# Performance work log

Measured on AMD Instinct MI355X. Metric: run time of the kernel, lower is better.

The kernel has to match this reference:

```python
import jax, jax.numpy as jnp
import numpy as np

H, KV, D, WIN = 16, 4, 128, 1024


def _rope(x, cos, sin):
    # x: [B, H, S, D]; cos/sin: [1, 1, S, D//2]
    d = x.shape[-1] // 2
    x1, x2 = x[..., :d], x[..., d:]
    S = x.shape[2]
    c, s = cos[:, :, :S], sin[:, :, :S]
    return jnp.concatenate([x1 * c + x2 * s, -x1 * s + x2 * c], axis=-1)


def _rms_norm(x):
    eps = jnp.finfo(x.dtype).eps
    return x * jax.lax.rsqrt(jnp.mean(jnp.square(x), axis=-1, keepdims=True) + eps)


def setup_inputs() -> dict:
    key = jax.random.key(0)
    ks = jax.random.split(key, 7)
    B, S, E = 2, 2048, 2048
    return {
        "x": jax.random.normal(ks[0], (B, S, E), jnp.float32),
        "cos": jax.random.normal(ks[1], (1, 1, S, D // 2), jnp.float32),
        "sin": jax.random.normal(ks[2], (1, 1, S, D // 2), jnp.float32),
        "Wq": jax.random.normal(ks[3], (H * D, E), jnp.float32) * 0.02,
        "Wk": jax.random.normal(ks[4], (KV * D, E), jnp.float32) * 0.02,
        "Wv": jax.random.normal(ks[5], (KV * D, E), jnp.float32) * 0.02,
        "Wo": jax.random.normal(ks[6], (E, H * D), jnp.float32) * 0.02,
    }


def reference(x, cos, sin, Wq, Wk, Wv, Wo):
    B, S, E = x.shape
    rep = H // KV
    # projections -> [B, heads, S, D]
    q = (x @ Wq.T).reshape(B, S, H, D).transpose(0, 2, 1, 3)
    k = (x @ Wk.T).reshape(B, S, KV, D).transpose(0, 2, 1, 3)
    v = (x @ Wv.T).reshape(B, S, KV, D).transpose(0, 2, 1, 3)
    # GQA: materialize repeated K/V heads (matches repeat_interleave)
    k = jnp.repeat(k, rep, axis=1)
    v = jnp.repeat(v, rep, axis=1)
    # RoPE then QK RMSNorm (no learned scale)
    q = _rms_norm(_rope(q, cos, sin))
    k = _rms_norm(_rope(k, cos, sin))
    scores = jnp.einsum("bhqd,bhkd->bhqk", q, k) * (D ** -0.5)
    # causal & sliding-window mask
    i = jnp.arange(S)[:, None]
    j = jnp.arange(S)[None, :]
    mask = (i >= j) & (jnp.abs(i - j) < WIN)
    scores = jnp.where(mask[None, None], scores, -jnp.inf)
    attn = jax.nn.softmax(scores, axis=-1)
    out = jnp.einsum("bhqk,bhkd->bhqd", attn, v)
    out = out.transpose(0, 2, 1, 3).reshape(B, S, H * D)
    return out @ Wo.T
```

## Files before the change

### kernel.cpp

```cpp
#include <hip/hip_runtime.h>
#include <stdint.h>

using bf16 = __bf16;
typedef __bf16 bf16x8 __attribute__((ext_vector_type(8)));
typedef __bf16 bf16x4 __attribute__((ext_vector_type(4)));
typedef float f32x4 __attribute__((ext_vector_type(4)));

#define H_ 16
#define KV_ 4
#define D_ 128
#define WIN_ 1024
#define B_ 2
#define S_ 2048
#define E_ 2048
#define HD_ 2048

__device__ __forceinline__ void gld_lds16(const void* gptr, void* lptr) {
    __builtin_amdgcn_global_load_lds(
        (__attribute__((address_space(1))) void*)(uintptr_t)gptr,
        (__attribute__((address_space(3))) void*)(uintptr_t)lptr, 16, 0, 0);
}

__global__ __launch_bounds__(256) void cvt_all(const float* __restrict__ x,
                                               const float* __restrict__ wq,
                                               const float* __restrict__ wk,
                                               const float* __restrict__ wv,
                                               const float* __restrict__ wo,
                                               bf16* __restrict__ dst) {
    int i = (blockIdx.x * 256 + threadIdx.x) * 4;
    const float* src;
    int off;
    if (i < 8388608)       { src = x;  off = 0; }
    else if (i < 12582912) { src = wq; off = 8388608; }
    else if (i < 13631488) { src = wk; off = 12582912; }
    else if (i < 14680064) { src = wv; off = 13631488; }
    else                   { src = wo; off = 14680064; }
    const float4 v = *(const float4*)(src + (i - off));
    bf16x4 o = {(bf16)v.x, (bf16)v.y, (bf16)v.z, (bf16)v.w};
    *(bf16x4*)(dst + i) = o;
}


#define SCHED0() __builtin_amdgcn_sched_barrier(0)
#define BAR()                          \
    do {                               \
        SCHED0();                      \
        __builtin_amdgcn_s_barrier();  \
        SCHED0();                      \
    } while (0)
#define WAITV(N) asm volatile("s_waitcnt vmcnt(" #N ")" ::: "memory")

#define MMA16(MH, NHI, BF)                                                          \
    do {                                                                            \
        __builtin_amdgcn_s_setprio(1);                                              \
        _Pragma("unroll") for (int kh_ = 0; kh_ < 2; ++kh_) {                       \
            _Pragma("unroll") for (int i_ = 0; i_ < 4; ++i_) {                      \
                _Pragma("unroll") for (int j_ = 0; j_ < 2; ++j_) {                  \
                    acc[(MH) * 4 + i_][(NHI) * 2 + j_] =                            \
                        __builtin_amdgcn_mfma_f32_16x16x32_bf16(                    \
                            af[i_][kh_], BF[j_][kh_],                               \
                            acc[(MH) * 4 + i_][(NHI) * 2 + j_], 0, 0, 0);           \
                }                                                                   \
            }                                                                       \
        }                                                                           \
        __builtin_amdgcn_s_setprio(0);                                              \
    } while (0)

#define TILE_NH2(TT, AC, BC, DOST, WC)                              \
    do {                                                            \
        rdA(AC, 0);                                                 \
        rdB(BC, 0, bf0);                                            \
        rdB(BC, 1, bf1);                                            \
        MMA16(0, 0, bf0);                                           \
        MMA16(0, 1, bf1);                                           \
        rdA(AC, 1);                                                 \
        MMA16(1, 0, bf0);                                           \
        MMA16(1, 1, bf1);                                           \
        BAR();                                                      \
        if (DOST) { stB((TT) + 2, BC); stA((TT) + 2, AC); }         \
        if ((WC) == 8) WAITV(8);                                    \
        else if ((WC) == 0) WAITV(0);                               \
        BAR();                                                      \
    } while (0)

#define TILE_NH1(TT, AC, BC, DOST, WC)                              \
    do {                                                            \
        rdA(AC, 0);                                                 \
        rdB(BC, 0, bf0);                                            \
        MMA16(0, 0, bf0);                                           \
        rdA(AC, 1);                                                 \
        MMA16(1, 0, bf0);                                           \
        BAR();                                                      \
        if (DOST) { stB((TT) + 2, BC); stA((TT) + 2, AC); }         \
        if ((WC) == 6) WAITV(6);                                    \
        else if ((WC) == 0) WAITV(0);                               \
        BAR();                                                      \
    } while (0)

template <int NH>
__device__ __forceinline__ void gemm_core(const bf16* __restrict__ A,
                                          const bf16* __restrict__ W, int K, int m0,
                                          int n0, bf16* sm, f32x4 (&acc)[8][2 * NH]) {
    const int t = threadIdx.x;
    const int lane = t & 63;
    const int wave = t >> 6;
    const int l15 = lane & 15;
    const int quad = lane >> 4;
    const int fsw8 = (l15 & 7) * 8;
    const int wm = (wave & 1) * 128;
    const int wn = (wave >> 1) * (NH * 32);
    const int nt = K >> 6;

    bf16* const As0 = sm;
    bf16* const As1 = sm + 16384;
    bf16* const Bs0 = sm + 32768;
    bf16* const Bs1 = Bs0 + NH * 8192;

    const int su = ((t & 7) ^ ((t >> 3) & 7)) * 8;
    const bf16* Ap = A + (size_t)(m0 + (t >> 3)) * K + su;
    const bf16* Wp = W + (size_t)(n0 + (t >> 3)) * K + su;

    auto stA = [&](int tt, bf16* dst) {
#pragma unroll
        for (int c = 0; c < 4; ++c)
            gld_lds16(Ap + tt * 64 + (size_t)(c * 64) * K, dst + c * 4096 + t * 8);
    };
    auto stB = [&](int tt, bf16* dst) {
#pragma unroll
        for (int c = 0; c < 2 * NH; ++c)
            gld_lds16(Wp + tt * 64 + (size_t)(c * 64) * K, dst + c * 4096 + t * 8);
    };

    bf16x8 af[4][2], bf0[2][2], bf1[2][2];
    auto rdA = [&](const bf16* S, int mh) {
#pragma unroll
        for (int i = 0; i < 4; ++i) {
            const bf16* r = &S[(wm + mh * 64 + i * 16 + l15) * 64];
#pragma unroll
            for (int kh = 0; kh < 2; ++kh)
                af[i][kh] = *(const bf16x8*)&r[((kh * 4 + quad) * 8) ^ fsw8];
        }
    };
    auto rdB = [&](const bf16* S, int nh, bf16x8 (&f)[2][2]) {
#pragma unroll
        for (int j = 0; j < 2; ++j) {
            const bf16* r = &S[(wn + nh * 32 + j * 16 + l15) * 64];
#pragma unroll
            for (int kh = 0; kh < 2; ++kh)
                f[j][kh] = *(const bf16x8*)&r[((kh * 4 + quad) * 8) ^ fsw8];
        }
    };

    stA(0, As0);
    stB(0, Bs0);
    stA(1, As1);
    stB(1, Bs1);
    SCHED0();
    if constexpr (NH == 2) WAITV(8);
    else WAITV(6);
    BAR();

    if constexpr (NH == 2) {
        for (int tt = 0; tt < nt - 2; tt += 2) {
            TILE_NH2(tt, As0, Bs0, 1, 8);
            TILE_NH2(tt + 1, As1, Bs1, 1, 8);
        }
        TILE_NH2(nt - 2, As0, Bs0, 0, 0);
        TILE_NH2(nt - 1, As1, Bs1, 0, -1);
    } else {
        for (int tt = 0; tt < nt - 2; tt += 2) {
            TILE_NH1(tt, As0, Bs0, 1, 6);
            TILE_NH1(tt + 1, As1, Bs1, 1, 6);
        }
        TILE_NH1(nt - 2, As0, Bs0, 0, 0);
        TILE_NH1(nt - 1, As1, Bs1, 0, -1);
    }
}

__global__ __launch_bounds__(512, 2) void gemm_qkv8(const bf16* __restrict__ A,
                                                    const bf16* __restrict__ W,
                                                    const float* __restrict__ cosp,
                                                    const float* __restrict__ sinp,
                                                    bf16* __restrict__ qn,
                                                    bf16* __restrict__ kn,
                                                    bf16* __restrict__ vt) {
    __shared__ alignas(16) bf16 sm[65536];
    const int flat = blockIdx.y * 16 + blockIdx.x;
    const int swz = (flat & 7) * 24 + (flat >> 3);
    const int m0 = (swz & 15) * 256;
    const int n0 = (swz >> 4) * 256;

    f32x4 acc[8][4] = {};
    gemm_core<2>(A, W, E_, m0, n0, sm, acc);

    const int t = threadIdx.x;
    const int lane = t & 63;
    const int wave = t >> 6;
    const int l15 = lane & 15;
    const int quad = lane >> 4;
    const int wm = (wave & 1) * 128;
    const int wn = (wave >> 1) * 64;
    bf16* Cs = sm;

#pragma unroll
    for (int ch = 0; ch < 2; ++ch) {
        __syncthreads();
        if (wm == ch * 128) {
#pragma unroll
            for (int mi = 0; mi < 8; ++mi) {
                const int rl = mi * 16 + quad * 4;
#pragma unroll
                for (int nf = 0; nf < 4; ++nf) {
                    const int col = wn + nf * 16 + l15;
#pragma unroll
                    for (int r = 0; r < 4; ++r)
                        Cs[(rl + r) * 264 + col] = (bf16)acc[mi][nf][r];
                }
            }
        }
        __syncthreads();

        if (n0 < 2560) {
            const int rt = t >> 1;
            const int row = rt & 127;
            const int hh = rt >> 7;
            const int half = t & 1;
            const int gr = m0 + ch * 128 + row;
            const int bb = gr >> 11;
            const int s = gr & 2047;
            const int unit = (n0 >> 7) + hh;
            const bf16* crow = &Cs[row * 264 + hh * 128 + half * 32];
            const float* cp = cosp + s * 64 + half * 32;
            const float* sp = sinp + s * 64 + half * 32;
            bf16x8 xa[4], xb2[4];
#pragma unroll
            for (int u = 0; u < 4; ++u) {
                xa[u] = *(const bf16x8*)(crow + u * 8);
                xb2[u] = *(const bf16x8*)(crow + 64 + u * 8);
            }
            float y1[32], y2[32], ss = 0.0f;
#pragma unroll
            for (int u = 0; u < 4; ++u)
#pragma unroll
                for (int e = 0; e < 8; ++e) {
                    const int jj = u * 8 + e;
                    const float x1 = (float)xa[u][e];
                    const float x2 = (float)xb2[u][e];
                    const float c = cp[jj];
                    const float sn = sp[jj];
                    y1[jj] = x1 * c + x2 * sn;
                    y2[jj] = x2 * c - x1 * sn;
                    ss += y1[jj] * y1[jj] + y2[jj] * y2[jj];
                }
            ss += __shfl_xor(ss, 1, 64);
            float rr = rsqrtf(ss * (1.0f / 128.0f) + 1.1920929e-7f);
            bf16* dst;
            if (unit < 16) {
                rr *= 0.12751740f;
                dst = qn + ((size_t)(bb * H_ + unit) * S_ + s) * 128 + half * 32;
            } else {
                dst = kn + ((size_t)(bb * KV_ + (unit - 16)) * S_ + s) * 128 + half * 32;
            }
#pragma unroll
            for (int u = 0; u < 4; ++u) {
                bf16x8 p1, p2;
#pragma unroll
                for (int e = 0; e < 8; ++e) {
                    p1[e] = (bf16)(y1[u * 8 + e] * rr);
                    p2[e] = (bf16)(y2[u * 8 + e] * rr);
                }
                *(bf16x8*)(dst + u * 8) = p1;
                *(bf16x8*)(dst + 64 + u * 8) = p2;
            }
        } else {
            const int hh = t >> 8;
            const int d = (t >> 1) & 127;
            const int sl0 = (t & 1) * 64;
            const int jv = (n0 >> 7) + hh - 20;
            const int base = m0 + ch * 128;
            const int bb = base >> 11;
            const int sW = (base & 2047) + sl0;
            bf16* vdst = vt + ((size_t)(bb * KV_ + jv) * 128 + d) * S_ + sW;
#pragma unroll
            for (int u = 0; u < 8; ++u) {
                bf16x8 pk;
#pragma unroll
                for (int e = 0; e < 8; ++e)
                    pk[e] = Cs[(sl0 + u * 8 + e) * 264 + hh * 128 + d];
                *(bf16x8*)(vdst + u * 8) = pk;
            }
        }
    }
}

__global__ __launch_bounds__(512, 2) void gemm_bt8(const bf16* __restrict__ A,
                                                   const bf16* __restrict__ W,
                                                   float* __restrict__ C, int K,
                                                   int ldc) {
    __shared__ alignas(16) bf16 sm[49152];
    const int flat = blockIdx.y * 16 + blockIdx.x;
    const int swz = (flat & 7) * 32 + (flat >> 3);
    const int m0 = (swz & 15) * 256;
    const int n0 = (swz >> 4) * 128;

    f32x4 acc[8][2] = {};
    gemm_core<1>(A, W, K, m0, n0, sm, acc);

    const int t = threadIdx.x;
    const int lane = t & 63;
    const int l15 = lane & 15;
    const int quad = lane >> 4;
    const int wave = t >> 6;
    const int wm = (wave & 1) * 128;
    const int wn = (wave >> 1) * 32;
#pragma unroll
    for (int mi = 0; mi < 8; ++mi) {
        const int row = m0 + wm + mi * 16 + quad * 4;
#pragma unroll
        for (int j = 0; j < 2; ++j) {
            const int col = n0 + wn + j * 16 + l15;
#pragma unroll
            for (int r = 0; r < 4; ++r) C[(size_t)(row + r) * ldc + col] = acc[mi][j][r];
        }
    }
}

__global__ __launch_bounds__(256, 4) void attn_fwd(const bf16* __restrict__ Qn,
                                                   const bf16* __restrict__ Kn,
                                                   const bf16* __restrict__ Vt,
                                                   bf16* __restrict__ Out) {
    __shared__ alignas(16) bf16 Ks[64 * 128];
    __shared__ alignas(16) bf16 Vs[128 * 64];
    __shared__ alignas(16) bf16 Ps[4 * 16 * 64];

    const int t = threadIdx.x;
    const int lane = t & 63;
    const int wave = t >> 6;
    const int l15 = lane & 15;
    const int quad = lane >> 4;
    const int swz = l15 & 7;
    const int qb0 = blockIdx.x * 64;
    const int h = blockIdx.y;
    const int b = blockIdx.z;
    const int hk = h >> 2;
    const int qw0 = qb0 + wave * 16;

    const bf16* qbase = Qn + ((size_t)((b * H_ + h) * S_) + qw0 + l15) * 128;
    bf16x8 qf[4];
#pragma unroll
    for (int c4 = 0; c4 < 4; ++c4) qf[c4] = *(const bf16x8*)(qbase + c4 * 32 + quad * 8);

    f32x4 o[8] = {};
    float m = -1e30f, lsum = 0.0f;

    const bf16* kroot = Kn + (size_t)((b * KV_ + hk) * S_) * 128;
    const bf16* vroot = Vt + (size_t)((b * KV_ + hk) * 128) * S_;

    const int ku = (t & 15) ^ ((t >> 4) & 7);
    const int krow = t >> 4;
    const int vu = (t & 7) ^ ((t >> 3) & 7);
    const int vrow = t >> 3;
    const bf16* kst = kroot + (size_t)krow * 128 + ku * 8;
    const bf16* vst = vroot + (size_t)vrow * S_ + vu * 8;
    bf16* ksl = &Ks[t * 8];
    bf16* vsl = &Vs[t * 8];

    int lo = qb0 - (WIN_ - 1);
    if (lo < 0) lo = 0;
    const int kb_start = lo & ~63;
    const int kb_end = qb0 + 64;

    for (int kb = kb_start; kb < kb_end; kb += 64) {
#pragma unroll
        for (int c = 0; c < 4; ++c) gld_lds16(kst + (size_t)(kb + c * 16) * 128, ksl + c * 2048);
#pragma unroll
        for (int c = 0; c < 4; ++c) gld_lds16(vst + (size_t)(c * 32) * S_ + kb, vsl + c * 2048);
        __syncthreads();

        const bool wave_active = (kb + 63 >= qw0 - (WIN_ - 1));
        if (wave_active) {
            f32x4 sacc[4] = {};
#pragma unroll
            for (int c4 = 0; c4 < 4; ++c4)
#pragma unroll
                for (int kblk = 0; kblk < 4; ++kblk) {
                    bf16x8 kf = *(const bf16x8*)&Ks[(kblk * 16 + l15) * 128 +
                                                    (((c4 * 4 + quad) ^ swz) * 8)];
                    sacc[kblk] =
                        __builtin_amdgcn_mfma_f32_16x16x32_bf16(kf, qf[c4], sacc[kblk], 0, 0, 0);
                }

            const int q = qw0 + l15;
            float sv[16];
            const bool interior = (kb + 63 <= qw0) && (kb >= qw0 + 15 - (WIN_ - 1));
            if (interior) {
#pragma unroll
                for (int kblk = 0; kblk < 4; ++kblk)
#pragma unroll
                    for (int r = 0; r < 4; ++r) sv[kblk * 4 + r] = sacc[kblk][r];
            } else {
#pragma unroll
                for (int kblk = 0; kblk < 4; ++kblk)
#pragma unroll
                    for (int r = 0; r < 4; ++r) {
                        const int key = kb + kblk * 16 + quad * 4 + r;
                        const bool valid = (key <= q) && (q - key < WIN_);
                        sv[kblk * 4 + r] = valid ? sacc[kblk][r] : -1e30f;
                    }
            }
            float mc = sv[0];
#pragma unroll
            for (int i = 1; i < 16; ++i) mc = fmaxf(mc, sv[i]);
            mc = fmaxf(mc, __shfl_xor(mc, 16, 64));
            mc = fmaxf(mc, __shfl_xor(mc, 32, 64));
            const float mnew = fmaxf(m, mc);
            const float al = __builtin_amdgcn_exp2f(m - mnew);
            float ls = 0.0f;
#pragma unroll
            for (int i = 0; i < 16; ++i) {
                sv[i] = __builtin_amdgcn_exp2f(sv[i] - mnew);
                ls += sv[i];
            }
            ls += __shfl_xor(ls, 16, 64);
            ls += __shfl_xor(ls, 32, 64);
            lsum = lsum * al + ls;
            m = mnew;
#pragma unroll
            for (int dblk = 0; dblk < 8; ++dblk) o[dblk] *= al;

            bf16* pw = &Ps[wave * 1024 + l15 * 64];
#pragma unroll
            for (int kblk = 0; kblk < 4; ++kblk) {
                bf16x4 pb = {(bf16)sv[kblk * 4 + 0], (bf16)sv[kblk * 4 + 1],
                             (bf16)sv[kblk * 4 + 2], (bf16)sv[kblk * 4 + 3]};
                const int phys = (kblk * 2 + (quad >> 1)) ^ swz;
                *(bf16x4*)&pw[phys * 8 + (quad & 1) * 4] = pb;
            }
#pragma unroll
            for (int kc = 0; kc < 2; ++kc) {
                const int up = ((kc * 4 + quad) ^ swz) * 8;
                bf16x8 pfv = *(const bf16x8*)&pw[up];
#pragma unroll
                for (int dblk = 0; dblk < 8; ++dblk) {
                    bf16x8 vf = *(const bf16x8*)&Vs[(dblk * 16 + l15) * 64 + up];
                    o[dblk] = __builtin_amdgcn_mfma_f32_16x16x32_bf16(vf, pfv, o[dblk], 0, 0, 0);
                }
            }
        }
        __syncthreads();
    }

    const float inv = 1.0f / lsum;
    const int q = qw0 + l15;
    bf16* ob = Out + (size_t)(b * S_ + q) * HD_ + h * 128;
#pragma unroll
    for (int dblk = 0; dblk < 8; ++dblk) {
        bf16x4 ov = {(bf16)(o[dblk][0] * inv), (bf16)(o[dblk][1] * inv),
                     (bf16)(o[dblk][2] * inv), (bf16)(o[dblk][3] * inv)};
        *(bf16x4*)&ob[dblk * 16 + quad * 4] = ov;
    }
}

extern "C" void kernel_launch(void* const* d_in, const int* in_sizes, int n_in, void* d_out,
                              int out_size, void* d_ws, size_t ws_size, hipStream_t stream) {
    const float* x = (const float*)d_in[0];
    const float* cosp = (const float*)d_in[1];
    const float* sinp = (const float*)d_in[2];
    const float* Wq = (const float*)d_in[3];
    const float* Wk = (const float*)d_in[4];
    const float* Wv = (const float*)d_in[5];
    const float* Wo = (const float*)d_in[6];
    float* out = (float*)d_out;

    constexpr size_t MB = 1ull << 20;
    char* ws = (char*)d_ws;
    bf16* xb    = (bf16*)(ws + 0);
    bf16* wqkv  = (bf16*)(ws + 16 * MB);
    bf16* wo    = (bf16*)(ws + 28 * MB);
    bf16* qn    = (bf16*)(ws + 40 * MB);
    bf16* kn    = (bf16*)(ws + 56 * MB);
    bf16* vt    = (bf16*)(ws + 60 * MB);
    bf16* attnb = (bf16*)(ws + 64 * MB);

    cvt_all<<<18432, 256, 0, stream>>>(x, Wq, Wk, Wv, Wo, xb);
    gemm_qkv8<<<dim3(16, 12), 512, 0, stream>>>(xb, wqkv, cosp, sinp, qn, kn, vt);
    attn_fwd<<<dim3(32, 16, 2), 256, 0, stream>>>(qn, kn, vt, attnb);
    gemm_bt8<<<dim3(16, 16), 512, 0, stream>>>(attnb, wo, out, 2048, 2048);
}
```

Measured before the change: 283.7 us.

## Double-buffer K/V LDS tiles in attention and raise MFMA wave priority

The attention kernel now keeps two LDS buffers for K and V and prefetches the next key block with async global-to-LDS loads while the current block is computed. This replaces the old load-then-sync pattern and needs only one barrier per iteration. It also wraps the MFMA sections in s_setprio. LDS use doubles, so the launch-bounds occupancy hint drops from 4 to 2 blocks per CU, which reduces latency hiding across waves.

```diff
diff --git a/kernel.cpp b/kernel.cpp
--- a/kernel.cpp
+++ b/kernel.cpp
@@ -39,7 +39,6 @@
     bf16x4 o = {(bf16)v.x, (bf16)v.y, (bf16)v.z, (bf16)v.w};
     *(bf16x4*)(dst + i) = o;
 }
-
 
 #define SCHED0() __builtin_amdgcn_sched_barrier(0)
 #define BAR()                          \
@@ -325,12 +324,12 @@
     }
 }
 
-__global__ __launch_bounds__(256, 4) void attn_fwd(const bf16* __restrict__ Qn,
+__global__ __launch_bounds__(256, 2) void attn_fwd(const bf16* __restrict__ Qn,
                                                    const bf16* __restrict__ Kn,
                                                    const bf16* __restrict__ Vt,
                                                    bf16* __restrict__ Out) {
-    __shared__ alignas(16) bf16 Ks[64 * 128];
-    __shared__ alignas(16) bf16 Vs[128 * 64];
+    __shared__ alignas(16) bf16 Ks[2][64 * 128];
+    __shared__ alignas(16) bf16 Vs[2][128 * 64];
     __shared__ alignas(16) bf16 Ps[4 * 16 * 64];
 
     const int t = threadIdx.x;
@@ -362,33 +361,47 @@
     const int vrow = t >> 3;
     const bf16* kst = kroot + (size_t)krow * 128 + ku * 8;
     const bf16* vst = vroot + (size_t)vrow * S_ + vu * 8;
-    bf16* ksl = &Ks[t * 8];
-    bf16* vsl = &Vs[t * 8];
+
+    auto stage = [&](int kb, int c) {
+        bf16* ksl = &Ks[c][t * 8];
+        bf16* vsl = &Vs[c][t * 8];
+#pragma unroll
+        for (int cc = 0; cc < 4; ++cc)
+            gld_lds16(kst + (size_t)(kb + cc * 16) * 128, ksl + cc * 2048);
+#pragma unroll
+        for (int cc = 0; cc < 4; ++cc)
+            gld_lds16(vst + (size_t)(cc * 32) * S_ + kb, vsl + cc * 2048);
+    };
 
     int lo = qb0 - (WIN_ - 1);
     if (lo < 0) lo = 0;
     const int kb_start = lo & ~63;
     const int kb_end = qb0 + 64;
 
+    stage(kb_start, 0);
+    WAITV(0);
+    __syncthreads();
+
+    int cur = 0;
     for (int kb = kb_start; kb < kb_end; kb += 64) {
-#pragma unroll
-        for (int c = 0; c < 4; ++c) gld_lds16(kst + (size_t)(kb + c * 16) * 128, ksl + c * 2048);
-#pragma unroll
-        for (int c = 0; c < 4; ++c) gld_lds16(vst + (size_t)(c * 32) * S_ + kb, vsl + c * 2048);
-        __syncthreads();
+        if (kb + 64 < kb_end) stage(kb + 64, cur ^ 1);
 
         const bool wave_active = (kb + 63 >= qw0 - (WIN_ - 1));
         if (wave_active) {
+            const bf16* Kc = &Ks[cur][0];
+            const bf16* Vc = &Vs[cur][0];
             f32x4 sacc[4] = {};
+            __builtin_amdgcn_s_setprio(1);
 #pragma unroll
             for (int c4 = 0; c4 < 4; ++c4)
 #pragma unroll
                 for (int kblk = 0; kblk < 4; ++kblk) {
-                    bf16x8 kf = *(const bf16x8*)&Ks[(kblk * 16 + l15) * 128 +
+                    bf16x8 kf = *(const bf16x8*)&Kc[(kblk * 16 + l15) * 128 +
                                                     (((c4 * 4 + quad) ^ swz) * 8)];
                     sacc[kblk] =
                         __builtin_amdgcn_mfma_f32_16x16x32_bf16(kf, qf[c4], sacc[kblk], 0, 0, 0);
                 }
+            __builtin_amdgcn_s_setprio(0);
 
             const int q = qw0 + l15;
             float sv[16];
@@ -436,18 +449,22 @@
                 const int phys = (kblk * 2 + (quad >> 1)) ^ swz;
                 *(bf16x4*)&pw[phys * 8 + (quad & 1) * 4] = pb;
             }
+            __builtin_amdgcn_s_setprio(1);
 #pragma unroll
             for (int kc = 0; kc < 2; ++kc) {
                 const int up = ((kc * 4 + quad) ^ swz) * 8;
                 bf16x8 pfv = *(const bf16x8*)&pw[up];
 #pragma unroll
                 for (int dblk = 0; dblk < 8; ++dblk) {
-                    bf16x8 vf = *(const bf16x8*)&Vs[(dblk * 16 + l15) * 64 + up];
+                    bf16x8 vf = *(const bf16x8*)&Vc[(dblk * 16 + l15) * 64 + up];
                     o[dblk] = __builtin_amdgcn_mfma_f32_16x16x32_bf16(vf, pfv, o[dblk], 0, 0, 0);
                 }
             }
-        }
+            __builtin_amdgcn_s_setprio(0);
+        }
+        WAITV(0);
         __syncthreads();
+        cur ^= 1;
     }
 
     const float inv = 1.0f / lsum;
```

After: 295.1 us. 1.04x slower.

## Restructure GEMM mainloop to 4-stage K=32 pipeline with register double-buffering

Applied to the files above, without the earlier changes.

Replaces the two-stage K=64 LDS pipeline with a four-stage ring of K=32 tiles and ping-pongs the A/B fragments between two register sets, so LDS reads for the next step overlap the current MFMA batch. The goal is to hide global-load and LDS latency better and to drop one barrier per step. K is now hardcoded to 2048. The XOR swizzle is removed, so the 32-wide rows (64-byte stride) may cause LDS bank conflicts, and the extra fragment registers raise register pressure under launch_bounds(512,2).

```diff
diff --git a/kernel.cpp b/kernel.cpp
--- a/kernel.cpp
+++ b/kernel.cpp
@@ -40,7 +40,6 @@
     *(bf16x4*)(dst + i) = o;
 }
 
-
 #define SCHED0() __builtin_amdgcn_sched_barrier(0)
 #define BAR()                          \
     do {                               \
@@ -50,131 +49,99 @@
     } while (0)
 #define WAITV(N) asm volatile("s_waitcnt vmcnt(" #N ")" ::: "memory")
 
-#define MMA16(MH, NHI, BF)                                                          \
-    do {                                                                            \
-        __builtin_amdgcn_s_setprio(1);                                              \
-        _Pragma("unroll") for (int kh_ = 0; kh_ < 2; ++kh_) {                       \
-            _Pragma("unroll") for (int i_ = 0; i_ < 4; ++i_) {                      \
-                _Pragma("unroll") for (int j_ = 0; j_ < 2; ++j_) {                  \
-                    acc[(MH) * 4 + i_][(NHI) * 2 + j_] =                            \
-                        __builtin_amdgcn_mfma_f32_16x16x32_bf16(                    \
-                            af[i_][kh_], BF[j_][kh_],                               \
-                            acc[(MH) * 4 + i_][(NHI) * 2 + j_], 0, 0, 0);           \
-                }                                                                   \
-            }                                                                       \
-        }                                                                           \
-        __builtin_amdgcn_s_setprio(0);                                              \
-    } while (0)
-
-#define TILE_NH2(TT, AC, BC, DOST, WC)                              \
-    do {                                                            \
-        rdA(AC, 0);                                                 \
-        rdB(BC, 0, bf0);                                            \
-        rdB(BC, 1, bf1);                                            \
-        MMA16(0, 0, bf0);                                           \
-        MMA16(0, 1, bf1);                                           \
-        rdA(AC, 1);                                                 \
-        MMA16(1, 0, bf0);                                           \
-        MMA16(1, 1, bf1);                                           \
-        BAR();                                                      \
-        if (DOST) { stB((TT) + 2, BC); stA((TT) + 2, AC); }         \
-        if ((WC) == 8) WAITV(8);                                    \
-        else if ((WC) == 0) WAITV(0);                               \
-        BAR();                                                      \
-    } while (0)
-
-#define TILE_NH1(TT, AC, BC, DOST, WC)                              \
-    do {                                                            \
-        rdA(AC, 0);                                                 \
-        rdB(BC, 0, bf0);                                            \
-        MMA16(0, 0, bf0);                                           \
-        rdA(AC, 1);                                                 \
-        MMA16(1, 0, bf0);                                           \
-        BAR();                                                      \
-        if (DOST) { stB((TT) + 2, BC); stA((TT) + 2, AC); }         \
-        if ((WC) == 6) WAITV(6);                                    \
-        else if ((WC) == 0) WAITV(0);                               \
-        BAR();                                                      \
-    } while (0)
 
 template <int NH>
-__device__ __forceinline__ void gemm_core(const bf16* __restrict__ A,
-                                          const bf16* __restrict__ W, int K, int m0,
-                                          int n0, bf16* sm, f32x4 (&acc)[8][2 * NH]) {
+__device__ __forceinline__ void gemm_core32(const bf16* __restrict__ A,
+                                            const bf16* __restrict__ W, int m0,
+                                            int n0, bf16* sm, f32x4 (&acc)[8][2 * NH]) {
+    constexpr int K = 2048;
     const int t = threadIdx.x;
     const int lane = t & 63;
     const int wave = t >> 6;
     const int l15 = lane & 15;
     const int quad = lane >> 4;
-    const int fsw8 = (l15 & 7) * 8;
     const int wm = (wave & 1) * 128;
     const int wn = (wave >> 1) * (NH * 32);
-    const int nt = K >> 6;
-
-    bf16* const As0 = sm;
-    bf16* const As1 = sm + 16384;
-    bf16* const Bs0 = sm + 32768;
-    bf16* const Bs1 = Bs0 + NH * 8192;
-
-    const int su = ((t & 7) ^ ((t >> 3) & 7)) * 8;
-    const bf16* Ap = A + (size_t)(m0 + (t >> 3)) * K + su;
-    const bf16* Wp = W + (size_t)(n0 + (t >> 3)) * K + su;
-
-    auto stA = [&](int tt, bf16* dst) {
-#pragma unroll
-        for (int c = 0; c < 4; ++c)
-            gld_lds16(Ap + tt * 64 + (size_t)(c * 64) * K, dst + c * 4096 + t * 8);
+
+    bf16* const A0 = sm;
+    bf16* const A1 = sm + 8192;
+    bf16* const A2 = sm + 16384;
+    bf16* const A3 = sm + 24576;
+    bf16* const B0 = sm + 32768;
+    bf16* const B1 = B0 + NH * 4096;
+    bf16* const B2 = B0 + NH * 8192;
+    bf16* const B3 = B0 + NH * 12288;
+
+    const bf16* Ap = A + (size_t)(m0 + (t >> 2)) * K + (t & 3) * 8;
+    const bf16* Wp = W + (size_t)(n0 + (t >> 2)) * K + (t & 3) * 8;
+
+    auto stA = [&](int u, bf16* d) {
+        gld_lds16(Ap + u * 32, d + t * 8);
+        gld_lds16(Ap + u * 32 + (size_t)128 * K, d + 4096 + t * 8);
     };
-    auto stB = [&](int tt, bf16* dst) {
-#pragma unroll
-        for (int c = 0; c < 2 * NH; ++c)
-            gld_lds16(Wp + tt * 64 + (size_t)(c * 64) * K, dst + c * 4096 + t * 8);
+    auto stB = [&](int u, bf16* d) {
+        gld_lds16(Wp + u * 32, d + t * 8);
+        if constexpr (NH == 2) gld_lds16(Wp + u * 32 + (size_t)128 * K, d + 4096 + t * 8);
     };
 
-    bf16x8 af[4][2], bf0[2][2], bf1[2][2];
-    auto rdA = [&](const bf16* S, int mh) {
-#pragma unroll
-        for (int i = 0; i < 4; ++i) {
-            const bf16* r = &S[(wm + mh * 64 + i * 16 + l15) * 64];
-#pragma unroll
-            for (int kh = 0; kh < 2; ++kh)
-                af[i][kh] = *(const bf16x8*)&r[((kh * 4 + quad) * 8) ^ fsw8];
-        }
+    bf16x8 afX[8], afY[8], bfX[2 * NH], bfY[2 * NH];
+    auto rdA = [&](const bf16* S, bf16x8 (&af)[8]) {
+#pragma unroll
+        for (int mi = 0; mi < 8; ++mi)
+            af[mi] = *(const bf16x8*)&S[(wm + mi * 16 + l15) * 32 + quad * 8];
     };
-    auto rdB = [&](const bf16* S, int nh, bf16x8 (&f)[2][2]) {
-#pragma unroll
-        for (int j = 0; j < 2; ++j) {
-            const bf16* r = &S[(wn + nh * 32 + j * 16 + l15) * 64];
-#pragma unroll
-            for (int kh = 0; kh < 2; ++kh)
-                f[j][kh] = *(const bf16x8*)&r[((kh * 4 + quad) * 8) ^ fsw8];
-        }
+    auto rdB = [&](const bf16* S, bf16x8 (&bf)[2 * NH]) {
+#pragma unroll
+        for (int j = 0; j < 2 * NH; ++j)
+            bf[j] = *(const bf16x8*)&S[(wn + j * 16 + l15) * 32 + quad * 8];
     };
-
-    stA(0, As0);
-    stB(0, Bs0);
-    stA(1, As1);
-    stB(1, Bs1);
+    auto MMA = [&](bf16x8 (&af)[8], bf16x8 (&bf)[2 * NH]) {
+        __builtin_amdgcn_s_setprio(1);
+#pragma unroll
+        for (int mi = 0; mi < 8; ++mi)
+#pragma unroll
+            for (int j = 0; j < 2 * NH; ++j)
+                acc[mi][j] = __builtin_amdgcn_mfma_f32_16x16x32_bf16(af[mi], bf[j],
+                                                                     acc[mi][j], 0, 0, 0);
+        __builtin_amdgcn_s_setprio(0);
+    };
+
+#define GT(U, AFM, BFM, AFR, BFR, RA, RB, SA, SB, DOST, WMODE)                      \
+    do {                                                                            \
+        if (DOST) { stA((U) + 3, SA); stB((U) + 3, SB); }                           \
+        MMA(AFM, BFM);                                                              \
+        rdA(RA, AFR);                                                               \
+        rdB(RB, BFR);                                                               \
+        SCHED0();                                                                   \
+        if ((WMODE) == 1) {                                                         \
+            if constexpr (NH == 2) { WAITV(4); } else { WAITV(3); }                 \
+        } else if ((WMODE) == 0) {                                                  \
+            WAITV(0);                                                               \
+        }                                                                           \
+        BAR();                                                                      \
+    } while (0)
+
+    stA(0, A0); stB(0, B0);
+    stA(1, A1); stB(1, B1);
+    stA(2, A2); stB(2, B2);
     SCHED0();
-    if constexpr (NH == 2) WAITV(8);
-    else WAITV(6);
+    if constexpr (NH == 2) { WAITV(4); } else { WAITV(3); }
     BAR();
-
-    if constexpr (NH == 2) {
-        for (int tt = 0; tt < nt - 2; tt += 2) {
-            TILE_NH2(tt, As0, Bs0, 1, 8);
-            TILE_NH2(tt + 1, As1, Bs1, 1, 8);
-        }
-        TILE_NH2(nt - 2, As0, Bs0, 0, 0);
-        TILE_NH2(nt - 1, As1, Bs1, 0, -1);
-    } else {
-        for (int tt = 0; tt < nt - 2; tt += 2) {
-            TILE_NH1(tt, As0, Bs0, 1, 6);
-            TILE_NH1(tt + 1, As1, Bs1, 1, 6);
-        }
-        TILE_NH1(nt - 2, As0, Bs0, 0, 0);
-        TILE_NH1(nt - 1, As1, Bs1, 0, -1);
+    rdA(A0, afX);
+    rdB(B0, bfX);
+
+    for (int it = 0; it < 15; ++it) {
+        const int u = it * 4;
+        GT(u + 0, afX, bfX, afY, bfY, A1, B1, A3, B3, 1, 1);
+        GT(u + 1, afY, bfY, afX, bfX, A2, B2, A0, B0, 1, 1);
+        GT(u + 2, afX, bfX, afY, bfY, A3, B3, A1, B1, 1, 1);
+        GT(u + 3, afY, bfY, afX, bfX, A0, B0, A2, B2, 1, 1);
     }
+    GT(60, afX, bfX, afY, bfY, A1, B1, A3, B3, 1, 1);
+    GT(61, afY, bfY, afX, bfX, A2, B2, A0, B0, 0, 0);
+    GT(62, afX, bfX, afY, bfY, A3, B3, A1, B1, 0, -1);
+    MMA(afY, bfY);
+#undef GT
 }
 
 __global__ __launch_bounds__(512, 2) void gemm_qkv8(const bf16* __restrict__ A,
@@ -191,7 +158,7 @@
     const int n0 = (swz >> 4) * 256;
 
     f32x4 acc[8][4] = {};
-    gemm_core<2>(A, W, E_, m0, n0, sm, acc);
+    gemm_core32<2>(A, W, m0, n0, sm, acc);
 
     const int t = threadIdx.x;
     const int lane = t & 63;
@@ -304,7 +271,7 @@
     const int n0 = (swz >> 4) * 128;
 
     f32x4 acc[8][2] = {};
-    gemm_core<1>(A, W, K, m0, n0, sm, acc);
+    gemm_core32<1>(A, W, m0, n0, sm, acc);
 
     const int t = threadIdx.x;
     const int lane = t & 63;
```

New measurement: 277.7 us. -2.1%, faster.
